# Kernel tuning notes

Hardware: AMD Instinct MI355X
Metric: run time of the kernel (lower is better)

## Reference

```python
import jax, jax.numpy as jnp
import numpy as np

N = 1_000_000      # total atoms
B = 1024           # number of molecules (batch segments)
NUM_ELEMENTS = 118
D_EMB = 64
D_HID = 128


def setup_inputs() -> dict:
    key = jax.random.key(0)
    ks = jax.random.split(key, 9)
    positions = jax.random.normal(ks[0], (N, 3), dtype=jnp.float32) * 5.0
    atomic_numbers = jax.random.randint(ks[1], (N,), 0, NUM_ELEMENTS, dtype=jnp.int64)
    batch = jnp.sort(jax.random.randint(ks[2], (N,), 0, B, dtype=jnp.int64))
    # learned parameters (torch Linear is y = x @ W.T + b; we store W as (in, out))
    embed = jax.random.normal(ks[3], (NUM_ELEMENTS, D_EMB), dtype=jnp.float32) * 0.1
    W1 = jax.random.normal(ks[4], (D_EMB, D_HID), dtype=jnp.float32) * (1.0 / np.sqrt(D_EMB))
    b1 = jnp.zeros((D_HID,), dtype=jnp.float32)
    W2 = jax.random.normal(ks[5], (D_HID, D_HID), dtype=jnp.float32) * (1.0 / np.sqrt(D_HID))
    b2 = jnp.zeros((D_HID,), dtype=jnp.float32)
    W3 = jax.random.normal(ks[6], (D_HID, 1), dtype=jnp.float32) * (1.0 / np.sqrt(D_HID))
    b3 = jnp.zeros((1,), dtype=jnp.float32)
    return {
        "positions": positions,
        "embed": embed,
        "W1": W1, "b1": b1,
        "W2": W2, "b2": b2,
        "W3": W3, "b3": b3,
        "atomic_numbers": atomic_numbers,
        "batch": batch,
    }


def reference(positions, embed, W1, b1, W2, b2, W3, b3, atomic_numbers, batch):
    def energy_fn(pos):
        h = embed[atomic_numbers]                       # [N, 64] gather
        pos_feat = jnp.sum(pos, axis=-1, keepdims=True) # [N, 1]
        h = h + 0.0 * pos_feat                          # keeps pos in the graph (grad is zero)
        x = jax.nn.silu(h @ W1 + b1)                    # [N, 128]
        x = jax.nn.silu(x @ W2 + b2)                    # [N, 128]
        per_atom = (x @ W3 + b3)[:, 0]                  # [N]
        # energy.scatter_add_(0, batch, per_atom)
        return jax.ops.segment_sum(per_atom, batch, num_segments=B)  # [B]

    energy = energy_fn(positions)
    # forces = -grad_R sum(V(R)); identically zero here but computed faithfully
    forces = -jax.grad(lambda p: energy_fn(p).sum())(positions)      # [N, 3]
    return (energy, forces)
```

## Files before the change

kernel.cpp:

```cpp
#include <hip/hip_runtime.h>

#define D_EMB   64
#define D_HID   128
#define NUM_EL  118
#define HPAD    120
#define NSLOT   4
#define CHUNK   1024
#define K1_GRID 2048

__global__ __launch_bounds__(256)
void mace_prep_kernel(const float* __restrict__ embed,
                      const float* __restrict__ W1, const float* __restrict__ b1,
                      const float* __restrict__ W2, const float* __restrict__ b2,
                      const float* __restrict__ W3, const float* __restrict__ b3,
                      const int* __restrict__ z,
                      const int* __restrict__ batch,
                      float* __restrict__ Etab,
                      int* __restrict__ starts,
                      int* __restrict__ chunkbase,
                      int* __restrict__ hist,
                      float4* __restrict__ forces4,
                      int nf4, int n, int B, int nchunk) {
    const int t   = threadIdx.x;
    const int bid = blockIdx.x;

    {
        const float4 z4f = make_float4(0.f, 0.f, 0.f, 0.f);
        for (int i = bid * 256 + t; i < nf4; i += K1_GRID * 256)
            forces4[i] = z4f;
    }

    if (bid < nchunk) {
        __shared__ unsigned int shist[NSLOT * HPAD];
        __shared__ int base_s;

        for (int i = t; i < NSLOT * HPAD; i += 256) shist[i] = 0u;

        const int n4 = n >> 2;
        const int i4 = (bid << 8) + t;
        const bool valid = (i4 < n4);
        int4 zv = make_int4(0,0,0,0), bv = make_int4(0,0,0,0);
        if (valid) {
            zv = ((const int4*)z)[i4];
            bv = ((const int4*)batch)[i4];
        }
        if (t == 0) base_s = bv.x;
        __syncthreads();
        const int base = base_s;

        if (valid) {
            const int s0 = bv.x - base, s1 = bv.y - base;
            const int s2 = bv.z - base, s3 = bv.w - base;
            if (s0 < NSLOT) atomicAdd(&shist[s0 * HPAD + zv.x], 1u);
            if (s1 < NSLOT) atomicAdd(&shist[s1 * HPAD + zv.y], 1u);
            if (s2 < NSLOT) atomicAdd(&shist[s2 * HPAD + zv.z], 1u);
            if (s3 < NSLOT) atomicAdd(&shist[s3 * HPAD + zv.w], 1u);

            const int idx = i4 << 2;
            if (bv.x != bv.y) { for (int b = bv.x + 1; b <= bv.y; ++b) starts[b] = idx + 1; }
            if (bv.y != bv.z) { for (int b = bv.y + 1; b <= bv.z; ++b) starts[b] = idx + 2; }
            if (bv.z != bv.w) { for (int b = bv.z + 1; b <= bv.w; ++b) starts[b] = idx + 3; }
            if (idx + 4 < n) {
                const int nx = batch[idx + 4];
                if (bv.w != nx) { for (int b = bv.w + 1; b <= nx; ++b) starts[b] = idx + 4; }
            }
        }
        if (t == 0) {
            chunkbase[bid] = base;
            if (bid == 0) {
                const int first = batch[0], last = batch[n - 1];
                for (int b = 0; b <= first; ++b) starts[b] = 0;
                for (int b = last + 1; b <= B; ++b) starts[b] = n;
            }
        }
        __syncthreads();

        int* __restrict__ hrow = hist + (size_t)bid * (NSLOT * HPAD);
        for (int i = t; i < NSLOT * HPAD; i += 256) hrow[i] = (int)shist[i];

    } else if (bid < nchunk + NUM_EL) {
        __shared__ float h[D_EMB];
        __shared__ float x1[D_HID];
        __shared__ float part[D_HID];
        __shared__ float wsum[2];
        const int zz = bid - nchunk;
        const int j  = t & 127;
        const int hf = t >> 7;

        if (t < D_EMB) h[t] = embed[zz * D_EMB + t];
        __syncthreads();

        {
            const int k0 = hf * 32;
            float a0 = 0.f, a1 = 0.f, a2 = 0.f, a3 = 0.f;
            #pragma unroll
            for (int k = 0; k < 32; k += 4) {
                a0 = fmaf(h[k0 + k + 0], W1[(k0 + k + 0) * D_HID + j], a0);
                a1 = fmaf(h[k0 + k + 1], W1[(k0 + k + 1) * D_HID + j], a1);
                a2 = fmaf(h[k0 + k + 2], W1[(k0 + k + 2) * D_HID + j], a2);
                a3 = fmaf(h[k0 + k + 3], W1[(k0 + k + 3) * D_HID + j], a3);
            }
            const float p = (a0 + a1) + (a2 + a3);
            if (hf == 1) part[j] = p;
            __syncthreads();
            if (hf == 0) {
                const float acc = b1[j] + p + part[j];
                x1[j] = acc / (1.0f + expf(-acc));
            }
            __syncthreads();
        }
        float r = 0.f;
        {
            const int k0 = hf * 64;
            float a0 = 0.f, a1 = 0.f, a2 = 0.f, a3 = 0.f;
            #pragma unroll
            for (int k = 0; k < 64; k += 4) {
                a0 = fmaf(x1[k0 + k + 0], W2[(k0 + k + 0) * D_HID + j], a0);
                a1 = fmaf(x1[k0 + k + 1], W2[(k0 + k + 1) * D_HID + j], a1);
                a2 = fmaf(x1[k0 + k + 2], W2[(k0 + k + 2) * D_HID + j], a2);
                a3 = fmaf(x1[k0 + k + 3], W2[(k0 + k + 3) * D_HID + j], a3);
            }
            const float p = (a0 + a1) + (a2 + a3);
            if (hf == 1) part[j] = p;
            __syncthreads();
            if (hf == 0) {
                const float acc2 = b2[j] + p + part[j];
                const float s2 = acc2 / (1.0f + expf(-acc2));
                r = s2 * W3[j];
            }
        }
        #pragma unroll
        for (int off = 32; off > 0; off >>= 1)
            r += __shfl_down(r, off, 64);
        if (hf == 0 && (t & 63) == 0) wsum[t >> 6] = r;
        __syncthreads();
        if (t == 0) Etab[zz] = wsum[0] + wsum[1] + b3[0];
    }
}

__global__ __launch_bounds__(256)
void mace_energy_kernel(const int* __restrict__ z,
                        const int* __restrict__ starts,
                        const int* __restrict__ chunkbase,
                        const int* __restrict__ hist,
                        const float* __restrict__ EtabG,
                        float* __restrict__ energy, int n) {
    __shared__ float etab_s[NUM_EL];
    __shared__ float wsum[4];
    const int b = blockIdx.x;
    const int t = threadIdx.x;

    if (t < NUM_EL) etab_s[t] = EtabG[t];
    const int start = starts[b];
    const int end   = starts[b + 1];
    __syncthreads();

    float acc = 0.f;
    if (end > start) {
        const int c0 = start >> 10;
        const int c1 = (end - 1) >> 10;
        for (int c = c0; c <= c1; ++c) {
            const int slot = b - chunkbase[c];
            if (slot < NSLOT) {
                if (t < NUM_EL) {
                    const int cnt = hist[((size_t)c * NSLOT + slot) * HPAD + t];
                    acc = fmaf((float)cnt, etab_s[t], acc);
                }
            } else {
                const int lo = max(start, c << 10);
                const int hi = min(end, (c + 1) << 10);
                for (int i = lo + t; i < hi; i += 256)
                    acc += etab_s[z[i]];
            }
        }
    }

    #pragma unroll
    for (int off = 32; off > 0; off >>= 1)
        acc += __shfl_down(acc, off, 64);
    if ((t & 63) == 0) wsum[t >> 6] = acc;
    __syncthreads();
    if (t == 0) energy[b] = (wsum[0] + wsum[1]) + (wsum[2] + wsum[3]);
}

extern "C" void kernel_launch(void* const* d_in, const int* in_sizes, int n_in,
                              void* d_out, int out_size, void* d_ws, size_t ws_size,
                              hipStream_t stream) {
    const float* embed = (const float*)d_in[1];
    const float* W1    = (const float*)d_in[2];
    const float* b1    = (const float*)d_in[3];
    const float* W2    = (const float*)d_in[4];
    const float* b2    = (const float*)d_in[5];
    const float* W3    = (const float*)d_in[6];
    const float* b3    = (const float*)d_in[7];
    const int*   zp    = (const int*)d_in[8];
    const int*   batch = (const int*)d_in[9];
    const int    n     = in_sizes[8];

    const int B      = out_size - 3 * n;
    const int nf4    = (3 * n) / 4;
    const int nchunk = (n + CHUNK - 1) / CHUNK;

    float*  energy  = (float*)d_out;
    float4* forces4 = (float4*)((float*)d_out + B);

    char* ws = (char*)d_ws;
    float* Etab      = (float*)(ws);
    int*   starts    = (int*)(ws + 512);
    int*   chunkbase = (int*)(ws + 8192);
    int*   hist      = (int*)(ws + 16384);

    mace_prep_kernel<<<K1_GRID, 256, 0, stream>>>(embed, W1, b1, W2, b2, W3, b3,
                                                  zp, batch, Etab, starts,
                                                  chunkbase, hist, forces4,
                                                  nf4, n, B, nchunk);
    mace_energy_kernel<<<B, 256, 0, stream>>>(zp, starts, chunkbase, hist,
                                              Etab, energy, n);
}
```

Baseline: 13.91 us.

## Shrink histogram to u16, reorder prep blocks, halve energy block size

```diff
diff --git a/kernel.cpp b/kernel.cpp
--- a/kernel.cpp
+++ b/kernel.cpp
@@ -6,7 +6,7 @@
 #define HPAD    120
 #define NSLOT   4
 #define CHUNK   1024
-#define K1_GRID 2048
+#define NCHUNK_BLOCKS(n) (((n) + CHUNK - 1) / CHUNK)
 
 __global__ __launch_bounds__(256)
 void mace_prep_kernel(const float* __restrict__ embed,
@@ -18,74 +18,32 @@
                       float* __restrict__ Etab,
                       int* __restrict__ starts,
                       int* __restrict__ chunkbase,
-                      int* __restrict__ hist,
+                      unsigned short* __restrict__ hist16,
                       float4* __restrict__ forces4,
-                      int nf4, int n, int B, int nchunk) {
+                      int nf4, int n, int B, int nblocks) {
     const int t   = threadIdx.x;
     const int bid = blockIdx.x;
 
     {
         const float4 z4f = make_float4(0.f, 0.f, 0.f, 0.f);
-        for (int i = bid * 256 + t; i < nf4; i += K1_GRID * 256)
+        const int stride = nblocks * 256;
+        for (int i = bid * 256 + t; i < nf4; i += stride)
             forces4[i] = z4f;
     }
 
-    if (bid < nchunk) {
-        __shared__ unsigned int shist[NSLOT * HPAD];
-        __shared__ int base_s;
-
-        for (int i = t; i < NSLOT * HPAD; i += 256) shist[i] = 0u;
-
-        const int n4 = n >> 2;
-        const int i4 = (bid << 8) + t;
-        const bool valid = (i4 < n4);
-        int4 zv = make_int4(0,0,0,0), bv = make_int4(0,0,0,0);
-        if (valid) {
-            zv = ((const int4*)z)[i4];
-            bv = ((const int4*)batch)[i4];
-        }
-        if (t == 0) base_s = bv.x;
-        __syncthreads();
-        const int base = base_s;
-
-        if (valid) {
-            const int s0 = bv.x - base, s1 = bv.y - base;
-            const int s2 = bv.z - base, s3 = bv.w - base;
-            if (s0 < NSLOT) atomicAdd(&shist[s0 * HPAD + zv.x], 1u);
-            if (s1 < NSLOT) atomicAdd(&shist[s1 * HPAD + zv.y], 1u);
-            if (s2 < NSLOT) atomicAdd(&shist[s2 * HPAD + zv.z], 1u);
-            if (s3 < NSLOT) atomicAdd(&shist[s3 * HPAD + zv.w], 1u);
-
-            const int idx = i4 << 2;
-            if (bv.x != bv.y) { for (int b = bv.x + 1; b <= bv.y; ++b) starts[b] = idx + 1; }
-            if (bv.y != bv.z) { for (int b = bv.y + 1; b <= bv.z; ++b) starts[b] = idx + 2; }
-            if (bv.z != bv.w) { for (int b = bv.z + 1; b <= bv.w; ++b) starts[b] = idx + 3; }
-            if (idx + 4 < n) {
-                const int nx = batch[idx + 4];
-                if (bv.w != nx) { for (int b = bv.w + 1; b <= nx; ++b) starts[b] = idx + 4; }
-            }
-        }
-        if (t == 0) {
-            chunkbase[bid] = base;
-            if (bid == 0) {
-                const int first = batch[0], last = batch[n - 1];
-                for (int b = 0; b <= first; ++b) starts[b] = 0;
-                for (int b = last + 1; b <= B; ++b) starts[b] = n;
-            }
-        }
-        __syncthreads();
-
-        int* __restrict__ hrow = hist + (size_t)bid * (NSLOT * HPAD);
-        for (int i = t; i < NSLOT * HPAD; i += 256) hrow[i] = (int)shist[i];
-
-    } else if (bid < nchunk + NUM_EL) {
+    if (bid < NUM_EL) {
         __shared__ float h[D_EMB];
         __shared__ float x1[D_HID];
         __shared__ float part[D_HID];
         __shared__ float wsum[2];
-        const int zz = bid - nchunk;
+        const int zz = bid;
         const int j  = t & 127;
         const int hf = t >> 7;
+
+        if (bid == 0 && t == 0) {
+            const int last = batch[n - 1];
+            for (int b = last + 1; b <= B; ++b) starts[b] = n;
+        }
 
         if (t < D_EMB) h[t] = embed[zz * D_EMB + t];
         __syncthreads();
@@ -135,18 +93,66 @@
         if (hf == 0 && (t & 63) == 0) wsum[t >> 6] = r;
         __syncthreads();
         if (t == 0) Etab[zz] = wsum[0] + wsum[1] + b3[0];
+
+    } else {
+        __shared__ unsigned int shist[NSLOT * HPAD];
+        __shared__ int lastw[256];
+        __shared__ int base_s;
+
+        const int c = bid - NUM_EL;
+        for (int i = t; i < NSLOT * HPAD; i += 256) shist[i] = 0u;
+
+        const int n4 = n >> 2;
+        const int i4 = (c << 8) + t;
+        const bool valid = (i4 < n4);
+        int4 zv = make_int4(0, 0, 0, 0), bv = make_int4(0, 0, 0, 0);
+        if (valid) {
+            zv = ((const int4*)z)[i4];
+            bv = ((const int4*)batch)[i4];
+        }
+        if (t == 0) base_s = bv.x;
+        lastw[t] = bv.w;
+        __syncthreads();
+        const int base = base_s;
+
+        if (valid) {
+            const int idx = i4 << 2;
+
+            const int s0 = bv.x - base, s1 = bv.y - base;
+            const int s2 = bv.z - base, s3 = bv.w - base;
+            if (s0 < NSLOT) atomicAdd(&shist[s0 * HPAD + zv.x], 1u);
+            if (s1 < NSLOT) atomicAdd(&shist[s1 * HPAD + zv.y], 1u);
+            if (s2 < NSLOT) atomicAdd(&shist[s2 * HPAD + zv.z], 1u);
+            if (s3 < NSLOT) atomicAdd(&shist[s3 * HPAD + zv.w], 1u);
+
+            int prev;
+            if (t > 0)            prev = lastw[t - 1];
+            else if (c > 0)       prev = batch[idx - 1];
+            else                  prev = -1;
+            if (prev != bv.x) { const int lo = (prev < 0) ? 0 : prev + 1;
+                                for (int b = lo; b <= bv.x; ++b) starts[b] = (prev < 0) ? 0 : idx; }
+            if (bv.x != bv.y) { for (int b = bv.x + 1; b <= bv.y; ++b) starts[b] = idx + 1; }
+            if (bv.y != bv.z) { for (int b = bv.y + 1; b <= bv.z; ++b) starts[b] = idx + 2; }
+            if (bv.z != bv.w) { for (int b = bv.z + 1; b <= bv.w; ++b) starts[b] = idx + 3; }
+        }
+        if (t == 0) chunkbase[c] = base;
+        __syncthreads();
+
+        unsigned short* __restrict__ hrow = hist16 + (size_t)c * (NSLOT * HPAD);
+        for (int i = t; i < NSLOT * HPAD; i += 256)
+            hrow[i] = (unsigned short)shist[i];
     }
 }
 
-__global__ __launch_bounds__(256)
+__global__ __launch_bounds__(128)
 void mace_energy_kernel(const int* __restrict__ z,
                         const int* __restrict__ starts,
                         const int* __restrict__ chunkbase,
-                        const int* __restrict__ hist,
+                        const unsigned short* __restrict__ hist16,
                         const float* __restrict__ EtabG,
                         float* __restrict__ energy, int n) {
     __shared__ float etab_s[NUM_EL];
-    __shared__ float wsum[4];
+    __shared__ float wsum[2];
     const int b = blockIdx.x;
     const int t = threadIdx.x;
 
@@ -163,13 +169,14 @@
             const int slot = b - chunkbase[c];
             if (slot < NSLOT) {
                 if (t < NUM_EL) {
-                    const int cnt = hist[((size_t)c * NSLOT + slot) * HPAD + t];
+                    const unsigned short cnt =
+                        hist16[((size_t)c * NSLOT + slot) * HPAD + t];
                     acc = fmaf((float)cnt, etab_s[t], acc);
                 }
             } else {
                 const int lo = max(start, c << 10);
                 const int hi = min(end, (c + 1) << 10);
-                for (int i = lo + t; i < hi; i += 256)
+                for (int i = lo + t; i < hi; i += 128)
                     acc += etab_s[z[i]];
             }
         }
@@ -180,7 +187,7 @@
         acc += __shfl_down(acc, off, 64);
     if ((t & 63) == 0) wsum[t >> 6] = acc;
     __syncthreads();
-    if (t == 0) energy[b] = (wsum[0] + wsum[1]) + (wsum[2] + wsum[3]);
+    if (t == 0) energy[b] = wsum[0] + wsum[1];
 }
 
 extern "C" void kernel_launch(void* const* d_in, const int* in_sizes, int n_in,
@@ -197,23 +204,24 @@
     const int*   batch = (const int*)d_in[9];
     const int    n     = in_sizes[8];
 
-    const int B      = out_size - 3 * n;
-    const int nf4    = (3 * n) / 4;
-    const int nchunk = (n + CHUNK - 1) / CHUNK;
+    const int B       = out_size - 3 * n;
+    const int nf4     = (3 * n) / 4;
+    const int nchunk  = NCHUNK_BLOCKS(n);
+    const int nblocks = NUM_EL + nchunk;
 
     float*  energy  = (float*)d_out;
     float4* forces4 = (float4*)((float*)d_out + B);
 
     char* ws = (char*)d_ws;
-    float* Etab      = (float*)(ws);
-    int*   starts    = (int*)(ws + 512);
-    int*   chunkbase = (int*)(ws + 8192);
-    int*   hist      = (int*)(ws + 16384);
-
-    mace_prep_kernel<<<K1_GRID, 256, 0, stream>>>(embed, W1, b1, W2, b2, W3, b3,
+    float*          Etab      = (float*)(ws);
+    int*            starts    = (int*)(ws + 512);
+    int*            chunkbase = (int*)(ws + 8192);
+    unsigned short* hist16    = (unsigned short*)(ws + 16384);
+
+    mace_prep_kernel<<<nblocks, 256, 0, stream>>>(embed, W1, b1, W2, b2, W3, b3,
                                                   zp, batch, Etab, starts,
-                                                  chunkbase, hist, forces4,
-                                                  nf4, n, B, nchunk);
-    mace_energy_kernel<<<B, 256, 0, stream>>>(zp, starts, chunkbase, hist,
+                                                  chunkbase, hist16, forces4,
+                                                  nf4, n, B, nblocks);
+    mace_energy_kernel<<<B, 128, 0, stream>>>(zp, starts, chunkbase, hist16,
                                               Etab, energy, n);
 }
```

Measured after the change: 13.79 us. About the same (-0.9%).
